# Optimization experiments

Measured on AMD Instinct MI355X. Metric: run time of the kernel, lower is better.

Reference implementation:

```python
import jax, jax.numpy as jnp
import numpy as np

C = 1.0        # curvature parameter (manifold curvature -1/C)
EPS = 1e-7


def expmap0_space(v, k):
    # v: [..., ds] spatial tangent vector at the hyperboloid origin (time comp 0)
    # returns ambient point [..., ds+1] = (sqrt(k)cosh(|v|/sqrt(k)), sqrt(k)sinh(|v|/sqrt(k)) v/|v|)
    sk = jnp.sqrt(k)
    n = jnp.maximum(jnp.linalg.norm(v, axis=-1, keepdims=True), EPS)
    t = sk * jnp.cosh(n / sk)
    s = sk * jnp.sinh(n / sk) * (v / n)
    return jnp.concatenate([t, s], axis=-1)


def logmap0_space(p, k):
    # p: [..., ds+1] hyperboloid point -> spatial tangent [..., ds] at origin
    sk = jnp.sqrt(k)
    t, s = p[..., :1], p[..., 1:]
    ns = jnp.maximum(jnp.linalg.norm(s, axis=-1, keepdims=True), EPS)
    d = sk * jnp.arccosh(jnp.maximum(t / sk, 1.0 + EPS))
    return d * (s / ns)


def setup_inputs() -> dict:
    key = jax.random.key(0)
    N, DS, E = 50000, 127, 800000
    ks = jax.random.split(key, 8)
    x = jax.random.normal(ks[0], (N, DS), dtype=jnp.float32) * 0.1
    edge_src = jax.random.randint(ks[1], (E,), 0, N)
    edge_dst = jax.random.randint(ks[2], (E,), 0, N)
    edge_weight = jax.random.uniform(ks[3], (E,), dtype=jnp.float32) / 16.0  # ~1/deg norm
    sc = 1.0 / np.sqrt(DS)
    W1 = jax.random.normal(ks[4], (DS, DS), dtype=jnp.float32) * sc
    b1 = jnp.zeros((DS,), dtype=jnp.float32)
    W2 = jax.random.normal(ks[5], (DS, DS), dtype=jnp.float32) * sc
    b2 = jnp.zeros((DS,), dtype=jnp.float32)
    return {"x": x, "W1": W1, "b1": b1, "W2": W2, "b2": b2,
            "edge_src": edge_src, "edge_dst": edge_dst, "edge_weight": edge_weight}


def reference(x, W1, b1, W2, b2, edge_src, edge_dst, edge_weight):
    N = x.shape[0]
    # encode(): cat zero time column + expmap0 onto hyperboloid
    p = expmap0_space(x, C)                 # [N, ds+1]
    h = logmap0_space(p, C)                 # tangent features at origin [N, ds]
    for (W, b) in ((W1, b1), (W2, b2)):
        # hyperbolic linear in tangent space
        z = h @ W + b                       # [N, ds]
        # adjacency-based neighbor aggregation (sparse spmm via edge list)
        msg = edge_weight[:, None] * z[edge_src]          # [E, ds] irregular gather
        agg = jax.ops.segment_sum(msg, edge_dst, num_segments=N)
        # activation + skip connection, back onto the manifold between layers
        h = jax.nn.relu(agg) + h
        h = logmap0_space(expmap0_space(h, C), C)
    return expmap0_space(h, C)              # [N, ds+1] on hyperboloid
```

## Files before the change

### kernel.cpp

```cpp
#include <hip/hip_runtime.h>

#define EPS 1e-7f
#define DS 127
#define DP 128
#define NBMAX 512
#define CAP 4096
#define CH 2048

typedef short bf16x8 __attribute__((ext_vector_type(8)));
typedef float f32x4  __attribute__((ext_vector_type(4)));
typedef float f32x2  __attribute__((ext_vector_type(2)));

__device__ __forceinline__ float wave_sum(float v) {
#pragma unroll
    for (int off = 32; off > 0; off >>= 1)
        v += __shfl_xor(v, off, 64);
    return v;
}

__device__ __forceinline__ unsigned short f2bf(float f) {
    unsigned u = __float_as_uint(f);
    unsigned r = (u + 0x7FFFu + ((u >> 16) & 1u)) >> 16;
    return (unsigned short)r;
}

__device__ __forceinline__ unsigned pack_bf2(float a, float b) {
    return (unsigned)f2bf(a) | ((unsigned)f2bf(b) << 16);
}

__device__ __forceinline__ unsigned char f2fp8(float v) {
    return (unsigned char)(__builtin_amdgcn_cvt_pk_fp8_f32(v, v, 0, false) & 0xFF);
}

__device__ __forceinline__ void sinhcosh(float n, float& sh, float& ch) {
    float e  = __expf(n);
    float em = __expf(-n);
    sh = 0.5f * (e - em);
    ch = 0.5f * (e + em);
}

__device__ __forceinline__ float logexp_scale(float n2) {
    float nrm = sqrtf(n2);
    float n   = fmaxf(nrm, EPS);
    float sh, ch;
    sinhcosh(n, sh, ch);
    float inv_n = 1.0f / n;
    float ns = fmaxf(sh * nrm * inv_n, EPS);
    float d  = (ch >= 1.0f + EPS) ? n : 4.472136e-4f;
    return d * sh * inv_n / ns;
}

__global__ void f_first_kernel(const float* __restrict__ x,
                               unsigned* __restrict__ hbu, int N) {
    int gw   = (int)((blockIdx.x * blockDim.x + threadIdx.x) >> 6);
    int lane = threadIdx.x & 63;
    if (gw >= N) return;

    const float* row = x + (size_t)gw * DS;
    float x0 = row[2 * lane];
    float x1 = (lane < 63) ? row[2 * lane + 1] : 0.f;

    float scale = logexp_scale(wave_sum(x0 * x0 + x1 * x1));

    float y0 = scale * x0;
    float y1 = (lane < 63) ? scale * x1 : 0.f;
    hbu[(size_t)gw * (DP / 2) + lane] = pack_bf2(y0, y1);
}

__global__ void padT_kernel(const float* __restrict__ W1, const float* __restrict__ b1,
                            unsigned short* __restrict__ Wt1, float* __restrict__ bp1,
                            const float* __restrict__ W2, const float* __restrict__ b2,
                            unsigned short* __restrict__ Wt2, float* __restrict__ bp2) {
    const float* W = blockIdx.y ? W2 : W1;
    const float* b = blockIdx.y ? b2 : b1;
    unsigned short* Wt = blockIdx.y ? Wt2 : Wt1;
    float* bp = blockIdx.y ? bp2 : bp1;
    int i = blockIdx.x * blockDim.x + threadIdx.x;
    if (i < DP * DP) {
        int n = i >> 7, k = i & (DP - 1);
        Wt[i] = (k < DS && n < DS) ? f2bf(W[k * DS + n]) : (unsigned short)0;
    } else if (i < DP * DP + DP) {
        int j = i - DP * DP;
        bp[j] = (j < DS) ? b[j] : 0.f;
    }
}

#define BM 64
__global__ __launch_bounds__(256) void gemm_mfma_kernel(
        const unsigned short* __restrict__ hb,
        const unsigned short* __restrict__ Wt,
        const float* __restrict__ bp,
        unsigned char* __restrict__ z8, int N) {
    int wave = threadIdx.x >> 6;
    int lane = threadIdx.x & 63;
    int m    = lane & 15;
    int quad = lane >> 4;
    int r0   = blockIdx.x * BM + wave * 16;

    f32x4 acc[8];
#pragma unroll
    for (int t = 0; t < 8; t++) acc[t] = (f32x4){0.f, 0.f, 0.f, 0.f};

    const bf16x8* arow = (const bf16x8*)(hb + (size_t)(r0 + m) * DP);
#pragma unroll
    for (int kq = 0; kq < 4; kq++) {
        bf16x8 a = arow[kq * 4 + quad];
#pragma unroll
        for (int nt = 0; nt < 8; nt++) {
            bf16x8 bfr = ((const bf16x8*)(Wt + (size_t)(nt * 16 + m) * DP))[kq * 4 + quad];
            acc[nt] = __builtin_amdgcn_mfma_f32_16x16x32_bf16(a, bfr, acc[nt], 0, 0, 0);
        }
    }

#pragma unroll
    for (int nt = 0; nt < 8; nt++) {
        float bias = bp[nt * 16 + m];
#pragma unroll
        for (int reg = 0; reg < 4; reg++) {
            int row = r0 + quad * 4 + reg;
            if (row < N)
                z8[(size_t)row * DP + nt * 16 + m] = f2fp8(acc[nt][reg] + bias);
        }
    }
}

__global__ __launch_bounds__(256) void binA_kernel(
        const int* __restrict__ es, const int* __restrict__ ed,
        const float* __restrict__ ew,
        int* __restrict__ gcnt, uint2* __restrict__ stg, int E) {
    __shared__ int  lcnt[NBMAX];
    __shared__ int  loff[NBMAX];
    __shared__ int  gbase[NBMAX];
    __shared__ uint2 lst[CH];

    int tid  = threadIdx.x;
    int lane = tid & 63;
    int base = blockIdx.x * CH;
    int cnt  = min(CH, E - base);

    for (int b = tid; b < NBMAX; b += 256) lcnt[b] = 0;
    __syncthreads();

    unsigned pk[CH / 256];
    int      rd[CH / 256];
#pragma unroll
    for (int k = 0; k < CH / 256; k++) {
        int i = base + k * 256 + tid;
        if (i < E) {
            int d = ed[i];
            rd[k] = d;
            pk[k] = ((unsigned)f2bf(ew[i]) << 16) | (unsigned)es[i];
            atomicAdd(&lcnt[d >> 7], 1);
        } else {
            rd[k] = -1;
        }
    }
    __syncthreads();

    if (tid < 64) {
        int carry = 0;
        for (int c = 0; c < NBMAX; c += 64) {
            int v = lcnt[c + lane];
            int inc = v;
#pragma unroll
            for (int off = 1; off < 64; off <<= 1) {
                int t = __shfl_up(inc, off, 64);
                if (lane >= off) inc += t;
            }
            loff[c + lane] = carry + inc - v;
            carry += __shfl(inc, 63, 64);
        }
    }
    __syncthreads();
    for (int b = tid; b < NBMAX; b += 256) lcnt[b] = 0;
    __syncthreads();

#pragma unroll
    for (int k = 0; k < CH / 256; k++) {
        if (rd[k] >= 0) {
            int b = rd[k] >> 7;
            int slot = loff[b] + atomicAdd(&lcnt[b], 1);
            lst[slot] = make_uint2(pk[k], (unsigned)rd[k]);
        }
    }
    __syncthreads();

    for (int b = tid; b < NBMAX; b += 256) {
        int c = lcnt[b];
        gbase[b] = c ? atomicAdd(&gcnt[b], c) : 0;
    }
    __syncthreads();

    for (int s = tid; s < cnt; s += 256) {
        uint2 u = lst[s];
        int b  = (int)(u.y >> 7);
        int li = s - loff[b];
        int idx = gbase[b] + li;
        if (idx >= CAP) idx = CAP - 1;
        stg[(size_t)b * CAP + idx] = u;
    }
}

__global__ void bscan_kernel(const int* __restrict__ gcnt, int nb,
                             int* __restrict__ bstart,
                             int* __restrict__ row_start, int N, int E) {
    int lane = threadIdx.x;
    int base = 0;
    for (int c = 0; c < nb; c += 64) {
        int idx = c + lane;
        int v = (idx < nb) ? min(gcnt[idx], CAP) : 0;
        int inc = v;
#pragma unroll
        for (int off = 1; off < 64; off <<= 1) {
            int t = __shfl_up(inc, off, 64);
            if (lane >= off) inc += t;
        }
        if (idx < nb) bstart[idx] = base + inc - v;
        base += __shfl(inc, 63, 64);
    }
    if (lane == 0) row_start[N] = E;
}

__global__ __launch_bounds__(256) void binB_kernel(
        const uint2* __restrict__ stg, const int* __restrict__ gcnt,
        const int* __restrict__ bstart,
        int* __restrict__ row_start, unsigned* __restrict__ epk, int N) {
    __shared__ int rcnt[128];
    __shared__ int roff[128];

    int b    = blockIdx.x;
    int tid  = threadIdx.x;
    int lane = tid & 63;
    int cnt  = min(gcnt[b], CAP);
    int bb   = bstart[b];
    const uint2* in = stg + (size_t)b * CAP;

    if (tid < 128) rcnt[tid] = 0;
    __syncthreads();

    for (int i = tid; i < cnt; i += 256)
        atomicAdd(&rcnt[in[i].y & 127u], 1);
    __syncthreads();

    if (tid < 64) {
        int carry = 0;
        for (int c = 0; c < 128; c += 64) {
            int v = rcnt[c + lane];
            int inc = v;
#pragma unroll
            for (int off = 1; off < 64; off <<= 1) {
                int t = __shfl_up(inc, off, 64);
                if (lane >= off) inc += t;
            }
            roff[c + lane] = carry + inc - v;
            carry += __shfl(inc, 63, 64);
        }
    }
    __syncthreads();

    if (tid < 128) {
        int row = b * 128 + tid;
        if (row < N) row_start[row] = bb + roff[tid];
        rcnt[tid] = 0;
    }
    __syncthreads();

    for (int i = tid; i < cnt; i += 256) {
        uint2 u = in[i];
        int r = (int)(u.y & 127u);
        int pos = atomicAdd(&rcnt[r], 1);
        epk[bb + roff[r] + pos] = u.x;
    }
}

template <bool LAST>
__global__ void agg_f_tpl(const unsigned char* __restrict__ zc,
                          const unsigned* __restrict__ hbu_in,
                          const int* __restrict__ row_start,
                          const unsigned* __restrict__ epk,
                          unsigned* __restrict__ hbu_out,
                          float* __restrict__ out, int N) {
    int gw   = (int)((blockIdx.x * blockDim.x + threadIdx.x) >> 6);
    int lane = threadIdx.x & 63;
    if (gw >= N) return;
    gw = __builtin_amdgcn_readfirstlane(gw);
    int lane2 = lane << 1;

    int beg = row_start[gw], end = row_start[gw + 1];
    float a0 = 0.f, a1 = 0.f;

    int e = beg;
    for (; e + 8 <= end; e += 8) {
        unsigned pks[8], us[8];
#pragma unroll
        for (int i = 0; i < 8; i++) pks[i] = epk[e + i];
#pragma unroll
        for (int i = 0; i < 8; i++)
            us[i] = *(const unsigned short*)(zc + (((pks[i] & 0xFFFFu) << 7) + lane2));
#pragma unroll
        for (int i = 0; i < 8; i++) {
            float wf = __uint_as_float(pks[i] & 0xFFFF0000u);
            f32x2 zv = __builtin_amdgcn_cvt_pk_f32_fp8(us[i], false);
            a0 = fmaf(wf, zv.x, a0);
            a1 = fmaf(wf, zv.y, a1);
        }
    }
    if (e < end) {
        int last = end - 1;
        unsigned pks[8], us[8];
#pragma unroll
        for (int i = 0; i < 8; i++) {
            int ei = e + i;
            unsigned p = epk[ei > last ? last : ei];
            if (ei > last) p &= 0xFFFFu;
            pks[i] = p;
        }
#pragma unroll
        for (int i = 0; i < 8; i++)
            us[i] = *(const unsigned short*)(zc + (((pks[i] & 0xFFFFu) << 7) + lane2));
#pragma unroll
        for (int i = 0; i < 8; i++) {
            float wf = __uint_as_float(pks[i] & 0xFFFF0000u);
            f32x2 zv = __builtin_amdgcn_cvt_pk_f32_fp8(us[i], false);
            a0 = fmaf(wf, zv.x, a0);
            a1 = fmaf(wf, zv.y, a1);
        }
    }

    unsigned hu = hbu_in[(size_t)gw * (DP / 2) + lane];
    float h0 = __uint_as_float(hu << 16);
    float h1 = __uint_as_float(hu & 0xFFFF0000u);
    float x0 = h0 + fmaxf(a0, 0.f);
    float x1 = (lane < 63) ? h1 + fmaxf(a1, 0.f) : 0.f;

    float scale = logexp_scale(wave_sum(x0 * x0 + x1 * x1));
    float y0 = scale * x0;
    float y1 = (lane < 63) ? scale * x1 : 0.f;

    if (!LAST) {
        hbu_out[(size_t)gw * (DP / 2) + lane] = pack_bf2(y0, y1);
    } else {
        float n2y = wave_sum(y0 * y0 + y1 * y1);
        float ny  = fmaxf(sqrtf(n2y), EPS);
        float shy, chy;
        sinhcosh(ny, shy, chy);
        float sc  = shy / ny;
        float* orow = out + (size_t)gw * DP;
        if (lane == 0) orow[0] = chy;
        orow[1 + 2 * lane] = sc * y0;
        if (lane < 63) orow[2 + 2 * lane] = sc * y1;
    }
}

extern "C" void kernel_launch(void* const* d_in, const int* in_sizes, int n_in,
                              void* d_out, int out_size, void* d_ws, size_t ws_size,
                              hipStream_t stream) {
    const float* x  = (const float*)d_in[0];
    const float* W1 = (const float*)d_in[1];
    const float* b1 = (const float*)d_in[2];
    const float* W2 = (const float*)d_in[3];
    const float* b2 = (const float*)d_in[4];
    const int*   es = (const int*)d_in[5];
    const int*   ed = (const int*)d_in[6];
    const float* ew = (const float*)d_in[7];

    const int N  = in_sizes[0] / DS;
    const int E  = in_sizes[5];
    const int NR = (N + BM - 1) / BM * BM;
    const int NB = (N + 127) >> 7;

    unsigned short* hb  = (unsigned short*)d_ws;
    unsigned char*  z8  = (unsigned char*)(hb + (size_t)NR * DP);
    unsigned short* Wt1 = (unsigned short*)(z8 + (size_t)N * DP);
    unsigned short* Wt2 = Wt1 + DP * DP;
    float* bp1          = (float*)(Wt2 + DP * DP);
    float* bp2          = bp1 + DP;
    unsigned* epk       = (unsigned*)(bp2 + DP);
    int*   row_start    = (int*)(epk + E);
    int*   gcnt         = row_start + N + 1;
    int*   bstart       = gcnt + NBMAX;
    uint2* stg          = (uint2*)((char*)(bstart + NBMAX) +
                          ((16 - ((size_t)(bstart + NBMAX) & 15)) & 15));

    unsigned* hbu = (unsigned*)hb;

    const int fBlocks    = (N * 64 + 255) / 256;
    const int gemmBlocks = (N + BM - 1) / BM;
    const int padBlocks  = (DP * DP + DP + 255) / 256;
    const int binABlocks = (E + CH - 1) / CH;

    hipMemsetAsync(gcnt, 0, NBMAX * sizeof(int), stream);
    binA_kernel<<<binABlocks, 256, 0, stream>>>(es, ed, ew, gcnt, stg, E);
    bscan_kernel<<<1, 64, 0, stream>>>(gcnt, NB, bstart, row_start, N, E);
    binB_kernel<<<NB, 256, 0, stream>>>(stg, gcnt, bstart, row_start, epk, N);

    padT_kernel<<<dim3(padBlocks, 2), 256, 0, stream>>>(W1, b1, Wt1, bp1,
                                                        W2, b2, Wt2, bp2);

    f_first_kernel<<<fBlocks, 256, 0, stream>>>(x, hbu, N);

    gemm_mfma_kernel<<<gemmBlocks, 256, 0, stream>>>(hb, Wt1, bp1, z8, N);
    agg_f_tpl<false><<<fBlocks, 256, 0, stream>>>(z8, hbu, row_start, epk,
                                                  hbu, nullptr, N);

    gemm_mfma_kernel<<<gemmBlocks, 256, 0, stream>>>(hb, Wt2, bp2, z8, N);
    agg_f_tpl<true><<<fBlocks, 256, 0, stream>>>(z8, hbu, row_start, epk,
                                                 nullptr, (float*)d_out, N);
}
```

Measured before the change: 235.2 us.

## Simplify logmap-expmap scale, shrink bin staging, unroll gather by 16

Replaces the sinh/cosh-based log(exp(h)) round-trip scale with a closed form: identity above a small norm threshold, clamp rescale below it. Splits the binning staging buffer into a 4-byte packed word plus a 1-byte row id, which cuts shared and global staging traffic. Adds a 16-wide gather stage in the aggregation loop to put more loads in flight. In the last layer it reuses the already computed norm instead of a second wave reduction. The closed-form scale drops the float rounding the original transcendental path had, so results can differ slightly.

```diff
diff --git a/kernel.cpp b/kernel.cpp
--- a/kernel.cpp
+++ b/kernel.cpp
@@ -32,6 +32,11 @@
     return (unsigned char)(__builtin_amdgcn_cvt_pk_fp8_f32(v, v, 0, false) & 0xFF);
 }
 
+__device__ __forceinline__ float logexp_scale(float n2) {
+    float nrm = sqrtf(n2);
+    return (nrm >= 4.472136e-4f) ? 1.0f : (4.472136e-4f / fmaxf(nrm, EPS));
+}
+
 __device__ __forceinline__ void sinhcosh(float n, float& sh, float& ch) {
     float e  = __expf(n);
     float em = __expf(-n);
@@ -39,17 +44,6 @@
     ch = 0.5f * (e + em);
 }
 
-__device__ __forceinline__ float logexp_scale(float n2) {
-    float nrm = sqrtf(n2);
-    float n   = fmaxf(nrm, EPS);
-    float sh, ch;
-    sinhcosh(n, sh, ch);
-    float inv_n = 1.0f / n;
-    float ns = fmaxf(sh * nrm * inv_n, EPS);
-    float d  = (ch >= 1.0f + EPS) ? n : 4.472136e-4f;
-    return d * sh * inv_n / ns;
-}
-
 __global__ void f_first_kernel(const float* __restrict__ x,
                                unsigned* __restrict__ hbu, int N) {
     int gw   = (int)((blockIdx.x * blockDim.x + threadIdx.x) >> 6);
@@ -61,10 +55,8 @@
     float x1 = (lane < 63) ? row[2 * lane + 1] : 0.f;
 
     float scale = logexp_scale(wave_sum(x0 * x0 + x1 * x1));
-
-    float y0 = scale * x0;
-    float y1 = (lane < 63) ? scale * x1 : 0.f;
-    hbu[(size_t)gw * (DP / 2) + lane] = pack_bf2(y0, y1);
+    hbu[(size_t)gw * (DP / 2) + lane] = pack_bf2(scale * x0,
+                                                 (lane < 63) ? scale * x1 : 0.f);
 }
 
 __global__ void padT_kernel(const float* __restrict__ W1, const float* __restrict__ b1,
@@ -127,11 +119,13 @@
 __global__ __launch_bounds__(256) void binA_kernel(
         const int* __restrict__ es, const int* __restrict__ ed,
         const float* __restrict__ ew,
-        int* __restrict__ gcnt, uint2* __restrict__ stg, int E) {
+        int* __restrict__ gcnt, unsigned* __restrict__ stg_pk,
+        unsigned char* __restrict__ stg_r, int E) {
     __shared__ int  lcnt[NBMAX];
     __shared__ int  loff[NBMAX];
     __shared__ int  gbase[NBMAX];
-    __shared__ uint2 lst[CH];
+    __shared__ unsigned       lst_pk[CH];
+    __shared__ unsigned short lst_d[CH];
 
     int tid  = threadIdx.x;
     int lane = tid & 63;
@@ -180,7 +174,8 @@
         if (rd[k] >= 0) {
             int b = rd[k] >> 7;
             int slot = loff[b] + atomicAdd(&lcnt[b], 1);
-            lst[slot] = make_uint2(pk[k], (unsigned)rd[k]);
+            lst_pk[slot] = pk[k];
+            lst_d[slot]  = (unsigned short)rd[k];
         }
     }
     __syncthreads();
@@ -192,12 +187,13 @@
     __syncthreads();
 
     for (int s = tid; s < cnt; s += 256) {
-        uint2 u = lst[s];
-        int b  = (int)(u.y >> 7);
-        int li = s - loff[b];
-        int idx = gbase[b] + li;
+        unsigned p = lst_pk[s];
+        int d = lst_d[s];
+        int b = d >> 7;
+        int idx = gbase[b] + (s - loff[b]);
         if (idx >= CAP) idx = CAP - 1;
-        stg[(size_t)b * CAP + idx] = u;
+        stg_pk[(size_t)b * CAP + idx] = p;
+        stg_r [(size_t)b * CAP + idx] = (unsigned char)(d & 127);
     }
 }
 
@@ -222,8 +218,8 @@
 }
 
 __global__ __launch_bounds__(256) void binB_kernel(
-        const uint2* __restrict__ stg, const int* __restrict__ gcnt,
-        const int* __restrict__ bstart,
+        const unsigned* __restrict__ stg_pk, const unsigned char* __restrict__ stg_r,
+        const int* __restrict__ gcnt, const int* __restrict__ bstart,
         int* __restrict__ row_start, unsigned* __restrict__ epk, int N) {
     __shared__ int rcnt[128];
     __shared__ int roff[128];
@@ -233,13 +229,14 @@
     int lane = tid & 63;
     int cnt  = min(gcnt[b], CAP);
     int bb   = bstart[b];
-    const uint2* in = stg + (size_t)b * CAP;
+    const unsigned*      in_pk = stg_pk + (size_t)b * CAP;
+    const unsigned char* in_r  = stg_r  + (size_t)b * CAP;
 
     if (tid < 128) rcnt[tid] = 0;
     __syncthreads();
 
     for (int i = tid; i < cnt; i += 256)
-        atomicAdd(&rcnt[in[i].y & 127u], 1);
+        atomicAdd(&rcnt[in_r[i]], 1);
     __syncthreads();
 
     if (tid < 64) {
@@ -266,12 +263,28 @@
     __syncthreads();
 
     for (int i = tid; i < cnt; i += 256) {
-        uint2 u = in[i];
-        int r = (int)(u.y & 127u);
+        int r = in_r[i];
         int pos = atomicAdd(&rcnt[r], 1);
-        epk[bb + roff[r] + pos] = u.x;
-    }
-}
+        epk[bb + roff[r] + pos] = in_pk[i];
+    }
+}
+
+#define GATHER(K)                                                             \
+    {                                                                         \
+        unsigned pks[K], us[K];                                               \
+        _Pragma("unroll")                                                     \
+        for (int i = 0; i < K; i++) pks[i] = epk[e + i];                      \
+        _Pragma("unroll")                                                     \
+        for (int i = 0; i < K; i++)                                           \
+            us[i] = *(const unsigned short*)(zc + (((pks[i] & 0xFFFFu) << 7) + lane2)); \
+        _Pragma("unroll")                                                     \
+        for (int i = 0; i < K; i++) {                                         \
+            float wf = __uint_as_float(pks[i] & 0xFFFF0000u);                 \
+            f32x2 zv = __builtin_amdgcn_cvt_pk_f32_fp8(us[i], false);         \
+            a0 = fmaf(wf, zv.x, a0);                                          \
+            a1 = fmaf(wf, zv.y, a1);                                          \
+        }                                                                     \
+    }
 
 template <bool LAST>
 __global__ void agg_f_tpl(const unsigned char* __restrict__ zc,
@@ -290,10 +303,18 @@
     float a0 = 0.f, a1 = 0.f;
 
     int e = beg;
-    for (; e + 8 <= end; e += 8) {
+    for (; e + 16 <= end; e += 16) GATHER(16)
+    for (; e + 8 <= end; e += 8)  GATHER(8)
+    if (e < end) {
+        int last = end - 1;
         unsigned pks[8], us[8];
 #pragma unroll
-        for (int i = 0; i < 8; i++) pks[i] = epk[e + i];
+        for (int i = 0; i < 8; i++) {
+            int ei = e + i;
+            unsigned p = epk[ei > last ? last : ei];
+            if (ei > last) p &= 0xFFFFu;
+            pks[i] = p;
+        }
 #pragma unroll
         for (int i = 0; i < 8; i++)
             us[i] = *(const unsigned short*)(zc + (((pks[i] & 0xFFFFu) << 7) + lane2));
@@ -305,42 +326,21 @@
             a1 = fmaf(wf, zv.y, a1);
         }
     }
-    if (e < end) {
-        int last = end - 1;
-        unsigned pks[8], us[8];
-#pragma unroll
-        for (int i = 0; i < 8; i++) {
-            int ei = e + i;
-            unsigned p = epk[ei > last ? last : ei];
-            if (ei > last) p &= 0xFFFFu;
-            pks[i] = p;
-        }
-#pragma unroll
-        for (int i = 0; i < 8; i++)
-            us[i] = *(const unsigned short*)(zc + (((pks[i] & 0xFFFFu) << 7) + lane2));
-#pragma unroll
-        for (int i = 0; i < 8; i++) {
-            float wf = __uint_as_float(pks[i] & 0xFFFF0000u);
-            f32x2 zv = __builtin_amdgcn_cvt_pk_f32_fp8(us[i], false);
-            a0 = fmaf(wf, zv.x, a0);
-            a1 = fmaf(wf, zv.y, a1);
-        }
-    }
 
     unsigned hu = hbu_in[(size_t)gw * (DP / 2) + lane];
-    float h0 = __uint_as_float(hu << 16);
-    float h1 = __uint_as_float(hu & 0xFFFF0000u);
-    float x0 = h0 + fmaxf(a0, 0.f);
-    float x1 = (lane < 63) ? h1 + fmaxf(a1, 0.f) : 0.f;
-
-    float scale = logexp_scale(wave_sum(x0 * x0 + x1 * x1));
+    float x0 = __uint_as_float(hu << 16) + fmaxf(a0, 0.f);
+    float x1 = (lane < 63) ? __uint_as_float(hu & 0xFFFF0000u) + fmaxf(a1, 0.f)
+                           : 0.f;
+
+    float n2 = wave_sum(x0 * x0 + x1 * x1);
+    float scale = logexp_scale(n2);
     float y0 = scale * x0;
     float y1 = (lane < 63) ? scale * x1 : 0.f;
 
     if (!LAST) {
         hbu_out[(size_t)gw * (DP / 2) + lane] = pack_bf2(y0, y1);
     } else {
-        float n2y = wave_sum(y0 * y0 + y1 * y1);
+        float n2y = scale * scale * n2;
         float ny  = fmaxf(sqrtf(n2y), EPS);
         float shy, chy;
         sinhcosh(ny, shy, chy);
@@ -379,8 +379,8 @@
     int*   row_start    = (int*)(epk + E);
     int*   gcnt         = row_start + N + 1;
     int*   bstart       = gcnt + NBMAX;
-    uint2* stg          = (uint2*)((char*)(bstart + NBMAX) +
-                          ((16 - ((size_t)(bstart + NBMAX) & 15)) & 15));
+    unsigned* stg_pk    = (unsigned*)(bstart + NBMAX);
+    unsigned char* stg_r = (unsigned char*)(stg_pk + (size_t)NBMAX * CAP);
 
     unsigned* hbu = (unsigned*)hb;
 
@@ -390,9 +390,10 @@
     const int binABlocks = (E + CH - 1) / CH;
 
     hipMemsetAsync(gcnt, 0, NBMAX * sizeof(int), stream);
-    binA_kernel<<<binABlocks, 256, 0, stream>>>(es, ed, ew, gcnt, stg, E);
+    binA_kernel<<<binABlocks, 256, 0, stream>>>(es, ed, ew, gcnt, stg_pk, stg_r, E);
     bscan_kernel<<<1, 64, 0, stream>>>(gcnt, NB, bstart, row_start, N, E);
-    binB_kernel<<<NB, 256, 0, stream>>>(stg, gcnt, bstart, row_start, epk, N);
+    binB_kernel<<<NB, 256, 0, stream>>>(stg_pk, stg_r, gcnt, bstart,
+                                        row_start, epk, N);
 
     padT_kernel<<<dim3(padBlocks, 2), 256, 0, stream>>>(W1, b1, Wt1, bp1,
                                                         W2, b2, Wt2, bp2);
```

Result: no change. 236.3 us (+0.4%).
